# Kernel optimization log

Hardware: AMD Instinct MI355X
Metric: run time of the kernel (lower is better)

The kernel has to match this reference:

```python
import jax, jax.numpy as jnp
import numpy as np

IMAGE_SIZE = 256
DET = int(IMAGE_SIZE * 2 ** 0.5 + 0.5)  # 362 detector bins (diagonal coverage)
US = 4
N_ACQ = 45                     # acquired views: 0,4,...,176 degrees
N_FULL = (N_ACQ - 1) * US + 1  # 177 full (upsampled) views


def setup_inputs() -> dict:
    key = jax.random.key(0)
    k1, k2 = jax.random.split(key)
    x_source = jax.random.normal(k1, (2, 1, IMAGE_SIZE, IMAGE_SIZE), jnp.float32)
    s_target = jax.random.normal(k2, (2, 1, DET, N_ACQ), jnp.float32)
    theta_acq = np.arange(0, 180, 4, dtype=np.float64)  # 45 acquired angles
    segs = [np.linspace(theta_acq[i], theta_acq[i + 1], US + 1)[:-1] for i in range(N_ACQ - 1)]
    theta_full = np.concatenate(segs + [theta_acq[-1:]]).astype(np.float32)  # [177]
    acq_idx = (np.arange(N_ACQ) * US).astype(np.int32)  # positions of acquired angles in theta_full
    return {"x_source": x_source, "s_target": s_target,
            "thetas_deg": jnp.asarray(theta_full), "acq_idx": jnp.asarray(acq_idx)}


def bilinear_gather(img, xs, ys):
    # img: [B,C,H,W]; xs, ys: pixel coords [A,det,det]; zero outside the image.
    H, W = img.shape[-2], img.shape[-1]
    x0 = jnp.floor(xs); y0 = jnp.floor(ys)
    wx = xs - x0; wy = ys - y0
    x0i = x0.astype(jnp.int32); y0i = y0.astype(jnp.int32)

    def get(yi, xi):
        valid = (xi >= 0) & (xi < W) & (yi >= 0) & (yi < H)
        v = img[:, :, jnp.clip(yi, 0, H - 1), jnp.clip(xi, 0, W - 1)]  # [B,C,A,det,det]
        return jnp.where(valid, v, 0.0)

    return (get(y0i, x0i) * (1 - wy) * (1 - wx)
            + get(y0i, x0i + 1) * (1 - wy) * wx
            + get(y0i + 1, x0i) * wy * (1 - wx)
            + get(y0i + 1, x0i + 1) * wy * wx)


def radon(x, thetas_rad, det):
    # Ray-sum projection: sino[theta, t] = sum_s image(t*cos - s*sin, t*sin + s*cos)
    B, C, H, W = x.shape
    t = jnp.arange(det, dtype=x.dtype) - (det - 1) / 2.0  # centered detector/ray coord
    cos = jnp.cos(thetas_rad)[:, None, None]
    sin = jnp.sin(thetas_rad)[:, None, None]
    T = t[None, :, None]; S = t[None, None, :]
    xs = T * cos - S * sin + (W - 1) / 2.0  # [A,det,det]
    ys = T * sin + S * cos + (H - 1) / 2.0
    return bilinear_gather(x, xs, ys).sum(-1)  # [B,C,A,det]


def ramp_filter(size):
    # skimage/pytorch_radon style ramp built from its real-space kernel
    n = np.concatenate([np.arange(1, size // 2 + 1, 2), np.arange(size // 2 - 1, 0, -2)])
    f = np.zeros(size)
    f[0] = 0.25
    f[1::2] = -1.0 / (np.pi * n) ** 2
    return jnp.asarray(2 * np.real(np.fft.fft(f)), dtype=jnp.float32)


def fbp(sino, thetas_rad, image_size):
    # Filtered back-projection. sino: [B,C,det,A]
    B, C, det, A = sino.shape
    pad = max(64, int(2 ** np.ceil(np.log2(2 * det))))
    filt = ramp_filter(pad)  # [pad]
    sp = jnp.pad(sino, ((0, 0), (0, 0), (0, pad - det), (0, 0)))
    sf = jnp.fft.ifft(jnp.fft.fft(sp, axis=2) * filt[None, None, :, None], axis=2).real
    sf = jnp.transpose(sf[:, :, :det, :], (0, 1, 3, 2)).astype(sino.dtype)  # [B,C,A,det]
    g = jnp.arange(image_size, dtype=sino.dtype) - (image_size - 1) / 2.0
    cos = jnp.cos(thetas_rad); sin = jnp.sin(thetas_rad)
    # detector coordinate hit by each pixel, per angle: t = x*cos + y*sin
    t = (cos[:, None, None] * g[None, None, :]
         + sin[:, None, None] * g[None, :, None] + (det - 1) / 2.0)  # [A,H,W]
    t = t.reshape(A, -1)
    t0 = jnp.floor(t)
    w = t - t0
    t0i = t0.astype(jnp.int32)
    aidx = jnp.arange(A)[:, None]

    def samp(ti):
        valid = (ti >= 0) & (ti < det)
        return jnp.where(valid, sf[:, :, aidx, jnp.clip(ti, 0, det - 1)], 0.0)  # [B,C,A,HW]

    v = samp(t0i) * (1 - w) + samp(t0i + 1) * w
    reco = v.sum(2) * (jnp.pi / (2 * A))
    return reco.reshape(B, C, image_size, image_size)


def reference(x_source, s_target, thetas_deg, acq_idx):
    th = thetas_deg * (jnp.pi / 180.0)
    s = radon(x_source, th, DET)          # [B,C,A,det]
    s = jnp.transpose(s, (0, 1, 3, 2))    # [B,C,det,A] -- angle axis last, as in the module
    # masked data-consistency update: acquired columns become (target - predicted)
    s = s.at[..., acq_idx].set(s_target - s[..., acq_idx])
    return fbp(s, th, IMAGE_SIZE)
```

## Files before the change

### kernel.cpp

```cpp
#include <hip/hip_runtime.h>
#include <math.h>

#define IMG   256
#define NFULL 177
#define DETN  362
#define NACQ  45
#define PAD   1024

#define SINO_OFF 0
#define SF_OFF   131072

#define HALF_T 180.5f
#define SEGL   16
#define TILE_W 640

__constant__ const int kStripOrd[46] =
    {22,23,21,24,20,25,19,26,18,27,17,28,16,29,15,30,14,31,13,32,
     12,33,11,34,10,35,9,36,8,37,7,38,6,39,5,40,4,41,3,42,2,43,1,44,0,45};

__device__ __forceinline__ void gload16(const float* g, float* l) {
    __builtin_amdgcn_global_load_lds(
        (const __attribute__((address_space(1))) void*)g,
        (__attribute__((address_space(3))) void*)l, 16, 0, 0);
}

template<int P>
__device__ __forceinline__ float2 radon_strip2(
    const float* __restrict__ img0,
    const float* __restrict__ img1,
    float* tb,
    const float c, const float s,
    const float xbase, const float ybase,
    const float xAB_mn, const float yAB_mn, const float yAB_mx,
    const int Slo, const int Shi, const int lane)
{
    constexpr int W4   = P / 4;
    constexpr int HMAX = TILE_W / P;
    const int ts = lane & 7;
    float val0 = 0.0f, val1 = 0.0f;

    for (int Sseg = Slo; Sseg < Shi; Sseg += SEGL) {
        const float sv0 = (float)Sseg - HALF_T;
        const float sv1 = sv0 + (float)(SEGL - 1);
        const float xmn = xAB_mn - sv1 * s;
        const float ya  = sv0 * c, yb = sv1 * c;
        const float ymn = yAB_mn + fminf(ya, yb);
        const float ymx = yAB_mx + fmaxf(ya, yb);
        const int ix0  = (int)floorf(xmn) - 1;
        const int iy0  = (int)floorf(ymn) - 1;
        const int ix0a = ix0 & ~3;
        const int h    = min((int)floorf(ymx) + 3 - iy0, HMAX);
        const int total4 = W4 * h;
        const int nfull  = total4 & ~63;
        const bool interior = (ix0a >= 0) & (iy0 >= 0) &
                              (ix0a + P <= IMG) & (iy0 + h <= IMG);

        asm volatile("s_waitcnt lgkmcnt(0)" ::: "memory");

        if (interior) {
            const int base0 = iy0 * IMG + ix0a;
            for (int f0 = 0; f0 < nfull; f0 += 64) {
                const int f  = f0 + lane;
                const int r  = f / W4;
                const int c4 = f - r * W4;
                const int go = base0 + r * IMG + (c4 << 2);
                gload16(img0 + go, tb + (f0 << 2));
                gload16(img1 + go, tb + TILE_W + (f0 << 2));
            }
            const int f = nfull + lane;
            if (f < total4) {
                const int r  = f / W4;
                const int c4 = f - r * W4;
                const int go = base0 + r * IMG + (c4 << 2);
                gload16(img0 + go, tb + (nfull << 2));
                gload16(img1 + go, tb + TILE_W + (nfull << 2));
            }
        } else {
            for (int f = lane; f < total4; f += 64) {
                const int r  = f / W4;
                const int c4 = f - r * W4;
                const int gy = iy0 + r;
                const int gx = ix0a + (c4 << 2);
                const bool ok = ((unsigned)gy < (unsigned)IMG) &
                                ((unsigned)gx <= (unsigned)(IMG - 4));
                float4 v0 = make_float4(0.f, 0.f, 0.f, 0.f);
                float4 v1 = v0;
                if (ok) {
                    const int go = gy * IMG + gx;
                    v0 = *(const float4*)(img0 + go);
                    v1 = *(const float4*)(img1 + go);
                }
                *(float4*)(tb + (f << 2)) = v0;
                *(float4*)(tb + TILE_W + (f << 2)) = v1;
            }
        }
        asm volatile("s_waitcnt vmcnt(0) lgkmcnt(0)" ::: "memory");
        __builtin_amdgcn_sched_barrier(0);

        const float xoff = xbase - (float)ix0a;
        const float yoff = ybase - (float)iy0;
        const int Send = min(Sseg + SEGL, Shi);

        auto samp = [&](float sval) {
            const float xs  = fmaf(-sval, s, xoff);
            const float ys  = fmaf(sval, c, yoff);
            const float x0f = floorf(xs);
            const float y0f = floorf(ys);
            const float wx  = xs - x0f;
            const float wy  = ys - y0f;
            const int base = (int)fmaf(y0f, (float)P, x0f);
            const float a00 = tb[base];
            const float a01 = tb[base + 1];
            const float a10 = tb[base + P];
            const float a11 = tb[base + P + 1];
            const float b00 = tb[TILE_W + base];
            const float b01 = tb[TILE_W + base + 1];
            const float b10 = tb[TILE_W + base + P];
            const float b11 = tb[TILE_W + base + P + 1];
            const float ah0 = fmaf(wx, a01 - a00, a00);
            const float ah1 = fmaf(wx, a11 - a10, a10);
            val0 += fmaf(wy, ah1 - ah0, ah0);
            const float bh0 = fmaf(wx, b01 - b00, b00);
            const float bh1 = fmaf(wx, b11 - b10, b10);
            val1 += fmaf(wy, bh1 - bh0, bh0);
        };

        if (Send - Sseg == SEGL) {
            const float s0 = (float)(Sseg + ts) - HALF_T;
            #pragma unroll
            for (int u = 0; u < SEGL / 8; ++u) samp(s0 + (float)(8 * u));
        } else {
            for (int S = Sseg + ts; S < Send; S += 8) samp((float)S - HALF_T);
        }
    }
    return make_float2(val0, val1);
}

__global__ __launch_bounds__(256, 8) void radon_kernel(
    const float* __restrict__ x,
    const float* __restrict__ thetas,
    float* __restrict__ sino)
{
    const int a = blockIdx.x;
    const int w    = threadIdx.x >> 6;
    const int lane = threadIdx.x & 63;
    const int sp   = kStripOrd[blockIdx.y];
    const int T0   = sp << 3;
    const int tt   = lane >> 3;
    const int ts   = lane & 7;
    const int T    = T0 + tt;

    __shared__ __align__(16) float tile[4][2 * TILE_W];
    float* tb = tile[w];

    const float th = thetas[a] * (float)(M_PI / 180.0);
    const float c = cosf(th);
    const float s = sinf(th);
    const float cx = (IMG - 1) * 0.5f;
    const float cy = (IMG - 1) * 0.5f;
    const float Tc = (float)T - HALF_T;
    const float xbase = Tc * c + cx;
    const float ybase = Tc * s + cy;

    float lo = -1e30f, hi = 1e30f;
    bool empty = (T >= DETN);
    {   const float aa = -s;
        if (aa > 1e-5f)       { lo = fmaxf(lo, (-1.0f - xbase) / aa); hi = fminf(hi, (256.0f - xbase) / aa); }
        else if (aa < -1e-5f) { lo = fmaxf(lo, (256.0f - xbase) / aa); hi = fminf(hi, (-1.0f - xbase) / aa); }
        else if (xbase <= -1.0f || xbase >= 256.0f) empty = true;
    }
    {   const float aa = c;
        if (aa > 1e-5f)       { lo = fmaxf(lo, (-1.0f - ybase) / aa); hi = fminf(hi, (256.0f - ybase) / aa); }
        else if (aa < -1e-5f) { lo = fmaxf(lo, (256.0f - ybase) / aa); hi = fminf(hi, (-1.0f - ybase) / aa); }
        else if (ybase <= -1.0f || ybase >= 256.0f) empty = true;
    }
    lo = fmaxf(lo, -200.0f);
    hi = fminf(hi, 200.0f);
    int Slo = max(0, (int)floorf(lo + HALF_T) - 1);
    int Shi = min(DETN, (int)floorf(hi + HALF_T) + 2);
    if (empty || Shi < Slo) { Slo = 0; Shi = 0; }

    int wlo = (Shi > Slo) ? Slo : DETN;
    int whi = (Shi > Slo) ? Shi : 0;
    #pragma unroll
    for (int d = 1; d < 64; d <<= 1) {
        wlo = min(wlo, __shfl_xor(wlo, d, 64));
        whi = max(whi, __shfl_xor(whi, d, 64));
    }

    const int range = max(whi - wlo, 0);
    const int nseg  = (range + SEGL - 1) / SEGL;
    const int per   = (nseg + 3) >> 2;
    const int q_lo  = wlo + w * per * SEGL;
    const int q_hi  = min(q_lo + per * SEGL, whi);

    int best = 2;
    {
        const float ac = fabsf(c), as = fabsf(s);
        const float spanx = 7.f * ac + 15.f * as;
        const float spany = 7.f * as + 15.f * ac;
        const float Pc[4] = {20.f, 24.f, 28.f, 32.f};
        const int   Hm[4] = {32, 26, 22, 20};
        int bcost = 1 << 30;
        #pragma unroll
        for (int p = 0; p < 4; ++p) {
            const float Pf = Pc[p];
            const float dT = s * Pf + c;
            const float dS = c * Pf - s;
            const int bank = (int)floorf((float)tt * dT + (float)ts * dS + 0.5f) & 31;
            unsigned long long m = ~0ull;
            #pragma unroll
            for (int bit = 0; bit < 5; ++bit) {
                const unsigned long long bb = __ballot((bank >> bit) & 1);
                m &= ((bank >> bit) & 1) ? bb : ~bb;
            }
            int cnt = __popcll(m);
            #pragma unroll
            for (int d = 1; d < 64; d <<= 1) cnt = max(cnt, __shfl_xor(cnt, d, 64));
            const bool fit = (spanx <= Pf - 8.05f) && (spany <= (float)Hm[p] - 5.05f);
            if (fit && cnt < bcost) { bcost = cnt; best = p; }
        }
    }

    const float TcA = (float)T0 - HALF_T;
    const float TcB = (float)(T0 + 7) - HALF_T;
    const float xAB_mn = fminf(TcA * c + cx, TcB * c + cx);
    const float yAB_mn = fminf(TcA * s + cy, TcB * s + cy);
    const float yAB_mx = fmaxf(TcA * s + cy, TcB * s + cy);

    const float* __restrict__ img0 = x;
    const float* __restrict__ img1 = x + IMG * IMG;

    float2 val;
    switch (best) {
    case 0:  val = radon_strip2<20>(img0, img1, tb, c, s, xbase, ybase,
                                    xAB_mn, yAB_mn, yAB_mx, q_lo, q_hi, lane); break;
    case 1:  val = radon_strip2<24>(img0, img1, tb, c, s, xbase, ybase,
                                    xAB_mn, yAB_mn, yAB_mx, q_lo, q_hi, lane); break;
    case 2:  val = radon_strip2<28>(img0, img1, tb, c, s, xbase, ybase,
                                    xAB_mn, yAB_mn, yAB_mx, q_lo, q_hi, lane); break;
    default: val = radon_strip2<32>(img0, img1, tb, c, s, xbase, ybase,
                                    xAB_mn, yAB_mn, yAB_mx, q_lo, q_hi, lane); break;
    }

    val.x += __shfl_xor(val.x, 1, 8);
    val.x += __shfl_xor(val.x, 2, 8);
    val.x += __shfl_xor(val.x, 4, 8);
    val.y += __shfl_xor(val.y, 1, 8);
    val.y += __shfl_xor(val.y, 2, 8);
    val.y += __shfl_xor(val.y, 4, 8);

    if (ts == 0) {
        tb[2 * tt]     = val.x;
        tb[2 * tt + 1] = val.y;
    }
    __syncthreads();
    if (w == 0 && lane < 16) {
        const float sum = tile[0][lane] + tile[1][lane]
                        + tile[2][lane] + tile[3][lane];
        const int T2 = T0 + (lane >> 1);
        const int bb = lane & 1;
        if (T2 < DETN) {
            sino[(bb * NFULL + a) * DETN + T2] = sum;
        }
    }
}

__global__ __launch_bounds__(192) void dc_filter_kernel(
    const float* __restrict__ sino,
    const float* __restrict__ st,
    const int*   __restrict__ acq,
    float* __restrict__ sf)
{
    const int blk = blockIdx.x;
    const int b = blk / NFULL;
    const int a = blk - b * NFULL;
    const int tid = threadIdx.x;

    __shared__ float col[DETN];
    __shared__ float gf[PAD];

    const float SC = (float)(M_PI / (2.0 * NFULL));
    const float c0 = 0.5f * SC;
    for (int n = tid; n < PAD; n += 192) {
        float v = 0.0f;
        if (n & 1) {
            const int d = (n < PAD - n) ? n : (PAD - n);
            const float pd = (float)M_PI * (float)d;
            v = -2.0f / (pd * pd) * SC;
        }
        gf[n] = v;
    }

    int inv = -1;
    for (int i = 0; i < NACQ; ++i) {
        if (acq[i] == a) inv = i;
    }

    for (int m = tid; m < DETN; m += 192) {
        float val = sino[(b * NFULL + a) * DETN + m];
        if (inv >= 0) {
            val = st[(b * DETN + m) * NACQ + inv] - val;
        }
        col[m] = val;
    }
    __syncthreads();

    const int T = blockIdx.y * 181 + tid;
    if (tid < 181) {
        const int m0 = (T + 1) & 1;
        float acc = c0 * col[T];
        #pragma unroll 4
        for (int k = 0; k < 181; ++k) {
            const int m = m0 + 2 * k;
            acc += col[m] * gf[(T - m) & (PAD - 1)];
        }
        sf[(b * NFULL + a) * DETN + T] = acc;
    }
}

__global__ __launch_bounds__(256) void backproject_kernel(
    const float* __restrict__ sf,
    const float* __restrict__ thetas,
    float* __restrict__ out)
{
    __shared__ float cb[2 * NFULL];
    __shared__ float red[256];
    const int tid = threadIdx.x;
    const int lane  = tid & 63;
    const int phase = tid >> 6;
    const int pix = blockIdx.x * 64 + lane;
    const int b = pix >> 16;
    const int y = (pix >> 8) & 255;
    const int xq = pix & 255;
    const float gx = (float)xq - (IMG - 1) * 0.5f;
    const float gy = (float)y  - (IMG - 1) * 0.5f;

    for (int a = tid; a < NFULL; a += 256) {
        float th = thetas[a] * (float)(M_PI / 180.0);
        cb[2 * a]     = cosf(th);
        cb[2 * a + 1] = fmaf(sinf(th), gy, HALF_T);
    }
    __syncthreads();

    const float* __restrict__ sfb = sf + b * NFULL * DETN;

    float acc = 0.0f;
    #pragma unroll 4
    for (int a = phase; a < NFULL; a += 4) {
        const float cs = cb[2 * a];
        const float bs = cb[2 * a + 1];
        const float t = fmaf(cs, gx, bs);
        const float t0f = floorf(t);
        const float w = t - t0f;
        const float* row = sfb + a * DETN + (int)t0f;
        const float v0 = row[0];
        const float v1 = row[1];
        acc += v0 + w * (v1 - v0);
    }
    red[tid] = acc;
    __syncthreads();
    if (tid < 64) {
        out[blockIdx.x * 64 + tid] =
            red[tid] + red[tid + 64] + red[tid + 128] + red[tid + 192];
    }
}

extern "C" void kernel_launch(void* const* d_in, const int* in_sizes, int n_in,
                              void* d_out, int out_size, void* d_ws, size_t ws_size,
                              hipStream_t stream) {
    const float* x      = (const float*)d_in[0];
    const float* st     = (const float*)d_in[1];
    const float* thetas = (const float*)d_in[2];
    const int*   acq    = (const int*)d_in[3];
    float* out  = (float*)d_out;
    float* wsf  = (float*)d_ws;
    float* sino = wsf + SINO_OFF;
    float* sf   = wsf + SF_OFF;

    dim3 gA(NFULL, 46);
    radon_kernel<<<gA, 256, 0, stream>>>(x, thetas, sino);
    dim3 gB(2 * NFULL, 2);
    dc_filter_kernel<<<gB, 192, 0, stream>>>(sino, st, acq, sf);
    backproject_kernel<<<(2 * IMG * IMG) / 64, 256, 0, stream>>>(sf, thetas, out);
}
```

Measured before the change: 122.7 us.

## Process two detector strips per radon block with two waves per strip

Each radon block now handles two 8-bin detector strips, with wave pairs splitting each strip's ray range in half instead of four waves splitting one strip, which halves the grid along y. The tile-pitch choice is narrowed from four candidates to two (24 and 28), reducing template instantiations and the ballot-based bank-conflict search. The final reduction sums two wave partials per strip. Intended to cut per-block setup overhead and code size, at the cost of fewer blocks and longer per-wave serial work, which may reduce load balance.

```diff
diff --git a/kernel.cpp b/kernel.cpp
--- a/kernel.cpp
+++ b/kernel.cpp
@@ -144,7 +144,8 @@
     const int a = blockIdx.x;
     const int w    = threadIdx.x >> 6;
     const int lane = threadIdx.x & 63;
-    const int sp   = kStripOrd[blockIdx.y];
+    const int sidx = (blockIdx.y << 1) | (w >> 1);
+    const int sp   = kStripOrd[sidx];
     const int T0   = sp << 3;
     const int tt   = lane >> 3;
     const int ts   = lane & 7;
@@ -190,20 +191,20 @@
 
     const int range = max(whi - wlo, 0);
     const int nseg  = (range + SEGL - 1) / SEGL;
-    const int per   = (nseg + 3) >> 2;
-    const int q_lo  = wlo + w * per * SEGL;
+    const int per   = (nseg + 1) >> 1;
+    const int q_lo  = wlo + (w & 1) * per * SEGL;
     const int q_hi  = min(q_lo + per * SEGL, whi);
 
-    int best = 2;
+    int best = 1;
     {
         const float ac = fabsf(c), as = fabsf(s);
         const float spanx = 7.f * ac + 15.f * as;
         const float spany = 7.f * as + 15.f * ac;
-        const float Pc[4] = {20.f, 24.f, 28.f, 32.f};
-        const int   Hm[4] = {32, 26, 22, 20};
+        const float Pc[2] = {24.f, 28.f};
+        const int   Hm[2] = {26, 22};
         int bcost = 1 << 30;
         #pragma unroll
-        for (int p = 0; p < 4; ++p) {
+        for (int p = 0; p < 2; ++p) {
             const float Pf = Pc[p];
             const float dT = s * Pf + c;
             const float dS = c * Pf - s;
@@ -232,15 +233,12 @@
     const float* __restrict__ img1 = x + IMG * IMG;
 
     float2 val;
-    switch (best) {
-    case 0:  val = radon_strip2<20>(img0, img1, tb, c, s, xbase, ybase,
-                                    xAB_mn, yAB_mn, yAB_mx, q_lo, q_hi, lane); break;
-    case 1:  val = radon_strip2<24>(img0, img1, tb, c, s, xbase, ybase,
-                                    xAB_mn, yAB_mn, yAB_mx, q_lo, q_hi, lane); break;
-    case 2:  val = radon_strip2<28>(img0, img1, tb, c, s, xbase, ybase,
-                                    xAB_mn, yAB_mn, yAB_mx, q_lo, q_hi, lane); break;
-    default: val = radon_strip2<32>(img0, img1, tb, c, s, xbase, ybase,
-                                    xAB_mn, yAB_mn, yAB_mx, q_lo, q_hi, lane); break;
+    if (best == 0) {
+        val = radon_strip2<24>(img0, img1, tb, c, s, xbase, ybase,
+                               xAB_mn, yAB_mn, yAB_mx, q_lo, q_hi, lane);
+    } else {
+        val = radon_strip2<28>(img0, img1, tb, c, s, xbase, ybase,
+                               xAB_mn, yAB_mn, yAB_mx, q_lo, q_hi, lane);
     }
 
     val.x += __shfl_xor(val.x, 1, 8);
@@ -255,11 +253,13 @@
         tb[2 * tt + 1] = val.y;
     }
     __syncthreads();
-    if (w == 0 && lane < 16) {
-        const float sum = tile[0][lane] + tile[1][lane]
-                        + tile[2][lane] + tile[3][lane];
-        const int T2 = T0 + (lane >> 1);
-        const int bb = lane & 1;
+    if (w == 0 && lane < 32) {
+        const int pair = lane >> 4;
+        const int k    = lane & 15;
+        const float sum = tile[2 * pair][k] + tile[2 * pair + 1][k];
+        const int spo = kStripOrd[(blockIdx.y << 1) | pair];
+        const int T2  = (spo << 3) + (k >> 1);
+        const int bb  = k & 1;
         if (T2 < DETN) {
             sino[(bb * NFULL + a) * DETN + T2] = sum;
         }
@@ -378,7 +378,7 @@
     float* sino = wsf + SINO_OFF;
     float* sf   = wsf + SF_OFF;
 
-    dim3 gA(NFULL, 46);
+    dim3 gA(NFULL, 23);
     radon_kernel<<<gA, 256, 0, stream>>>(x, thetas, sino);
     dim3 gB(2 * NFULL, 2);
     dc_filter_kernel<<<gB, 192, 0, stream>>>(sino, st, acq, sf);
```

Result: faster. 111.6 us (-9.1%).
